# Performance work log

Measured on AMD Instinct MI355X. Metric: run time of the kernel, lower is better.

The kernel has to match this reference:

```python
import jax, jax.numpy as jnp
import numpy as np

B, S, D, H, DFF = 8, 1024, 1024, 16, 4096
DK = D // H
EPS = 1e-5


def layernorm(x, g, b):
    mu = jnp.mean(x, axis=-1, keepdims=True)
    var = jnp.var(x, axis=-1, keepdims=True)
    return (x - mu) * jax.lax.rsqrt(var + EPS) * g + b


def mha(q_in, k_in, v_in, wq, bq, wk, bk, wv, bv, wo, bo):
    # weights stored as [in, out] (transposed torch Linear)
    nb = q_in.shape[0]
    def split(t):  # [B,S,D] -> [B,H,S,DK]
        return t.reshape(nb, -1, H, DK).transpose(0, 2, 1, 3)
    q = split(q_in @ wq + bq)
    k = split(k_in @ wk + bk)
    v = split(v_in @ wv + bv)
    scores = jnp.einsum('bhqd,bhkd->bhqk', q, k) / jnp.sqrt(jnp.float32(DK))
    p = jax.nn.softmax(scores, axis=-1)
    o = jnp.einsum('bhqk,bhkd->bhqd', p, v)
    o = o.transpose(0, 2, 1, 3).reshape(nb, -1, D)
    return o @ wo + bo


def setup_inputs() -> dict:
    key = jax.random.key(0)
    ks = jax.random.split(key, 40)
    i = iter(range(40))
    def rn(shape, scale=1.0):
        return jax.random.normal(ks[next(i)], shape, dtype=jnp.float32) * scale
    d = {}
    d['x'] = rn((B, S, D))
    d['y'] = rn((B, S, D))
    d['x_pos'] = rn((B, S, D))
    d['y_pos'] = rn((B, S, D))
    w_scale = 1.0 / np.sqrt(D)
    for pfx in ('sa', 'ca'):
        for nm in ('q', 'k', 'v', 'o'):
            d[f'{pfx}_w{nm}'] = rn((D, D), w_scale)
            d[f'{pfx}_b{nm}'] = jnp.zeros((D,), jnp.float32)
    d['ffn_w1'] = rn((D, DFF), w_scale)
    d['ffn_b1'] = jnp.zeros((DFF,), jnp.float32)
    d['ffn_w2'] = rn((DFF, D), 1.0 / np.sqrt(DFF))
    d['ffn_b2'] = jnp.zeros((D,), jnp.float32)
    for n in (1, 2, 3, 4):
        d[f'ln{n}_g'] = jnp.ones((D,), jnp.float32)
        d[f'ln{n}_b'] = jnp.zeros((D,), jnp.float32)
    return d


def reference(x, y, x_pos, y_pos,
              sa_wq, sa_bq, sa_wk, sa_bk, sa_wv, sa_bv, sa_wo, sa_bo,
              ca_wq, ca_bq, ca_wk, ca_bk, ca_wv, ca_bv, ca_wo, ca_bo,
              ffn_w1, ffn_b1, ffn_w2, ffn_b2,
              ln1_g, ln1_b, ln2_g, ln2_b, ln3_g, ln3_b, ln4_g, ln4_b):
    # pre-norm variant (norm_before=True), eval mode (dropout=0)
    x2 = layernorm(x, ln1_g, ln1_b)
    qk = x2 + x_pos
    x = x + mha(qk, qk, x2, sa_wq, sa_bq, sa_wk, sa_bk, sa_wv, sa_bv, sa_wo, sa_bo)
    x2 = layernorm(x, ln2_g, ln2_b)
    y2 = layernorm(y, ln3_g, ln3_b)
    x = x + mha(x2 + x_pos, y2 + y_pos, y2,
                ca_wq, ca_bq, ca_wk, ca_bk, ca_wv, ca_bv, ca_wo, ca_bo)
    x2 = layernorm(x, ln4_g, ln4_b)
    h = x2 @ ffn_w1 + ffn_b1
    h = h * jax.nn.sigmoid(h)  # Swish
    return x + (h @ ffn_w2 + ffn_b2)
```

## Files before the change

### kernel.cpp

```cpp
#include <hip/hip_runtime.h>
#include <hip/hip_bf16.h>

#define NB 8
#define NS 1024
#define ND 1024
#define NH 16
#define NDK 64
#define NDFF 4096

typedef __bf16 bf16;
typedef __attribute__((ext_vector_type(8))) __bf16 bf16x8;
typedef __attribute__((ext_vector_type(4))) __bf16 bf16x4;
typedef __attribute__((ext_vector_type(4))) float f32x4;

__device__ __forceinline__ void gload16(const bf16* g, bf16* l) {
  __builtin_amdgcn_global_load_lds(
      (const __attribute__((address_space(1))) void*)g,
      (__attribute__((address_space(3))) void*)l, 16, 0, 0);
}

__global__ void wconv_t(const float* __restrict__ W, bf16* __restrict__ WT,
                        int K, int N) {
  __shared__ float tile[32][33];
  int n0 = blockIdx.x * 32, k0 = blockIdx.y * 32;
  int tx = threadIdx.x, ty = threadIdx.y;
#pragma unroll
  for (int i2 = 0; i2 < 4; ++i2) {
    int i = ty + i2 * 8;
    tile[i][tx] = W[(long)(k0 + i) * N + n0 + tx];
  }
  __syncthreads();
#pragma unroll
  for (int i2 = 0; i2 < 4; ++i2) {
    int i = ty + i2 * 8;
    WT[(long)(n0 + i) * K + k0 + tx] = (bf16)tile[tx][i];
  }
}

__global__ void ln_fused(const float* __restrict__ in, const float* __restrict__ gam,
                         const float* __restrict__ bet, const float* __restrict__ pos,
                         bf16* __restrict__ out_ln, bf16* __restrict__ out_lnpos) {
  long row = blockIdx.x;
  int t = threadIdx.x;
  float4 v = ((const float4*)(in + row * ND))[t];
  float s = v.x + v.y + v.z + v.w;
  float s2 = v.x * v.x + v.y * v.y + v.z * v.z + v.w * v.w;
#pragma unroll
  for (int m = 32; m >= 1; m >>= 1) {
    s += __shfl_xor(s, m);
    s2 += __shfl_xor(s2, m);
  }
  __shared__ float red[8];
  if ((t & 63) == 0) {
    red[t >> 6] = s;
    red[4 + (t >> 6)] = s2;
  }
  __syncthreads();
  float ts = red[0] + red[1] + red[2] + red[3];
  float ts2 = red[4] + red[5] + red[6] + red[7];
  float mu = ts * (1.0f / ND);
  float var = ts2 * (1.0f / ND) - mu * mu;
  float rstd = rsqrtf(var + 1e-5f);
  float4 g4 = ((const float4*)gam)[t];
  float4 b4 = ((const float4*)bet)[t];
  float o0 = (v.x - mu) * rstd * g4.x + b4.x;
  float o1 = (v.y - mu) * rstd * g4.y + b4.y;
  float o2 = (v.z - mu) * rstd * g4.z + b4.z;
  float o3 = (v.w - mu) * rstd * g4.w + b4.w;
  if (out_ln) {
    bf16x4 q;
    q[0] = (bf16)o0; q[1] = (bf16)o1; q[2] = (bf16)o2; q[3] = (bf16)o3;
    *(bf16x4*)(out_ln + row * ND + t * 4) = q;
  }
  if (out_lnpos) {
    float4 p4 = ((const float4*)(pos + row * ND))[t];
    bf16x4 q;
    q[0] = (bf16)(o0 + p4.x); q[1] = (bf16)(o1 + p4.y);
    q[2] = (bf16)(o2 + p4.z); q[3] = (bf16)(o3 + p4.w);
    *(bf16x4*)(out_lnpos + row * ND + t * 4) = q;
  }
}

template <int MODE>
__global__ __launch_bounds__(512, 2) void gemm_bt(
    const bf16* __restrict__ A, const bf16* __restrict__ WT,
    const float* __restrict__ bias, const float* __restrict__ res,
    void* __restrict__ out, int M, int N, int K) {
  __shared__ bf16 SA[5][256 * 32];
  __shared__ bf16 SB[5][128 * 32];
  const int t = threadIdx.x;
  const int w = t >> 6, l = t & 63;
  const int wr = w >> 2, wc = w & 3;
  const int wrm = w >> 1, wcn = w & 1;
  (void)wr; (void)wc;
  const int c = l & 15, g = l >> 4;
  const long row0 = (long)blockIdx.x * 256;
  const long col0 = (long)blockIdx.y * 128;
  const int NT = K >> 5;

  f32x4 acc[4][4];
#pragma unroll
  for (int m = 0; m < 4; ++m)
#pragma unroll
    for (int n = 0; n < 4; ++n) acc[m][n] = (f32x4){0.f, 0.f, 0.f, 0.f};

  const int lr = l >> 2;
  const int lcol = 8 * ((l & 3) ^ ((l >> 3) & 3));
  const bf16* Ag0 = A + (row0 + w * 32 + lr) * (long)K + lcol;
  const bf16* Ag1 = Ag0 + 16 * (long)K;
  const bf16* Bg0 = WT + (col0 + w * 16 + lr) * (long)K + lcol;

#define STAGE(BS, KK)                              \
  do {                                             \
    gload16(Ag0 + (KK), &SA[BS][(w * 32) * 32]);   \
    gload16(Ag1 + (KK), &SA[BS][(w * 32 + 16) * 32]); \
    gload16(Bg0 + (KK), &SB[BS][(w * 16) * 32]);   \
  } while (0)

  STAGE(0, 0);
  STAGE(1, 32);
  STAGE(2, 64);
  STAGE(3, 96);

  const int swz8 = (g ^ ((c >> 1) & 3)) * 8;
  int aoff[4], boff[4];
#pragma unroll
  for (int m = 0; m < 4; ++m) aoff[m] = (wrm * 64 + m * 16 + c) * 32 + swz8;
#pragma unroll
  for (int n = 0; n < 4; ++n) boff[n] = (wcn * 64 + n * 16 + c) * 32 + swz8;

  int cb = 0, sb = 4;
  int ks_off = 128;
  for (int tt = 0; tt < NT; ++tt) {
    const int rem = NT - 1 - tt;
    if (rem >= 3) {
      asm volatile("s_waitcnt vmcnt(9)" ::: "memory");
    } else if (rem == 2) {
      asm volatile("s_waitcnt vmcnt(6)" ::: "memory");
    } else if (rem == 1) {
      asm volatile("s_waitcnt vmcnt(3)" ::: "memory");
    } else {
      asm volatile("s_waitcnt vmcnt(0)" ::: "memory");
    }
    __builtin_amdgcn_s_barrier();

    const int ca = cb * (256 * 32);
    const int cbb = cb * (128 * 32);
    bf16x8 af[4], bfr[4];
#pragma unroll
    for (int m = 0; m < 4; ++m) af[m] = *(const bf16x8*)&SA[0][ca + aoff[m]];
#pragma unroll
    for (int n = 0; n < 4; ++n) bfr[n] = *(const bf16x8*)&SB[0][cbb + boff[n]];

    if (tt + 4 < NT) STAGE(sb, ks_off);

    __builtin_amdgcn_s_barrier();
    __builtin_amdgcn_s_setprio(1);
#pragma unroll
    for (int m = 0; m < 4; ++m)
#pragma unroll
      for (int n = 0; n < 4; ++n)
        acc[m][n] = __builtin_amdgcn_mfma_f32_16x16x32_bf16(af[m], bfr[n], acc[m][n], 0, 0, 0);
    __builtin_amdgcn_s_setprio(0);

    cb = (cb == 4) ? 0 : cb + 1;
    sb = (sb == 4) ? 0 : sb + 1;
    ks_off += 32;
  }
#undef STAGE

#pragma unroll
  for (int n = 0; n < 4; ++n) {
    const long col = col0 + wcn * 64 + n * 16 + c;
    const float bv = bias[col];
#pragma unroll
    for (int m = 0; m < 4; ++m) {
      const long rowb = row0 + wrm * 64 + m * 16 + g * 4;
#pragma unroll
      for (int r = 0; r < 4; ++r) {
        float v = acc[m][n][r] + bv;
        const long idx = (rowb + r) * N + col;
        if (MODE == 0) {
          ((bf16*)out)[idx] = (bf16)v;
        } else if (MODE == 1) {
          ((float*)out)[idx] = res[idx] + v;
        } else {
          float sw = v / (1.f + __expf(-v));
          ((bf16*)out)[idx] = (bf16)sw;
        }
      }
    }
  }
}

__global__ void vtrans(const bf16* __restrict__ V, bf16* __restrict__ VT) {
  __shared__ bf16 tile[32][33];
  int st = blockIdx.x * 32, dt = blockIdx.y * 32;
  int bh = blockIdx.z;
  int b = bh >> 4, h = bh & 15;
  int tx = threadIdx.x, ty = threadIdx.y;
#pragma unroll
  for (int i2 = 0; i2 < 4; ++i2) {
    int i = ty + i2 * 8;
    tile[i][tx] = V[((long)b * NS + st + i) * ND + h * NDK + dt + tx];
  }
  __syncthreads();
#pragma unroll
  for (int i2 = 0; i2 < 4; ++i2) {
    int i = ty + i2 * 8;
    VT[((long)bh * NDK + dt + i) * NS + st + tx] = tile[tx][i];
  }
}

__global__ __launch_bounds__(256) void attn_fwd(
    const bf16* __restrict__ Q, const bf16* __restrict__ Kt,
    const bf16* __restrict__ VT, bf16* __restrict__ O) {
  __shared__ bf16 Ks[2][64 * 64];
  __shared__ bf16 Vs[2][64 * 64];
  __shared__ bf16 Pl[4][2][16 * 68];
  int t = threadIdx.x;
  int w = t >> 6, l = t & 63;
  int c = l & 15, g = l >> 4;
  int bid = blockIdx.x;
  int qt = bid >> 7, bh = bid & 127;
  int b = bh >> 4, h = bh & 15;
  int q0 = qt * 128 + w * 32;
  int swz = (c & 7) << 4;

  bf16x8 qf[2][2];
  const bf16* Qbase = Q + (long)(b * NS) * ND + h * NDK;
#pragma unroll
  for (int sj = 0; sj < 2; ++sj) {
    const bf16* qr = Qbase + (long)(q0 + sj * 16 + c) * ND + g * 8;
    qf[sj][0] = *(const bf16x8*)qr;
    qf[sj][1] = *(const bf16x8*)(qr + 32);
  }

  const bf16* Kg = Kt + (long)(b * NS) * ND + h * NDK;
  const bf16* Vg = VT + (long)(b * NH + h) * NDK * NS;

  int sr = l >> 3;
  int sc8 = 8 * ((l & 7) ^ sr);

  f32x4 o[2][4];
#pragma unroll
  for (int sj = 0; sj < 2; ++sj)
#pragma unroll
    for (int ds = 0; ds < 4; ++ds) o[sj][ds] = (f32x4){0.f, 0.f, 0.f, 0.f};
  float mx[2] = {-1e30f, -1e30f};
  float lsum[2] = {0.f, 0.f};

#define STAGE(BUF, KV)                                                        \
  {                                                                           \
    _Pragma("unroll") for (int j = 0; j < 2; ++j) {                           \
      int row = w * 16 + j * 8 + sr;                                          \
      gload16(Kg + (long)((KV) + row) * ND + sc8,                             \
              &Ks[BUF][(w * 16 + j * 8) * 64]);                               \
      gload16(Vg + (long)row * NS + (KV) + sc8,                               \
              &Vs[BUF][(w * 16 + j * 8) * 64]);                               \
    }                                                                         \
  }

  STAGE(0, 0);
  asm volatile("s_waitcnt vmcnt(0)" ::: "memory");
  __syncthreads();

  int buf = 0;
  for (int it = 0; it < NS / 64; ++it) {
    if (it + 1 < NS / 64) STAGE(buf ^ 1, (it + 1) * 64);

    f32x4 sv[2][4];
#pragma unroll
    for (int sj = 0; sj < 2; ++sj)
#pragma unroll
      for (int kt = 0; kt < 4; ++kt) sv[sj][kt] = (f32x4){0.f, 0.f, 0.f, 0.f};
    __builtin_amdgcn_s_setprio(1);
#pragma unroll
    for (int kt = 0; kt < 4; ++kt) {
      const char* kr = (const char*)&Ks[buf][(kt * 16 + c) * 64];
      bf16x8 ka0 = *(const bf16x8*)(kr + ((g * 16) ^ swz));
      bf16x8 ka1 = *(const bf16x8*)(kr + ((64 + g * 16) ^ swz));
#pragma unroll
      for (int sj = 0; sj < 2; ++sj) {
        sv[sj][kt] = __builtin_amdgcn_mfma_f32_16x16x32_bf16(ka0, qf[sj][0], sv[sj][kt], 0, 0, 0);
        sv[sj][kt] = __builtin_amdgcn_mfma_f32_16x16x32_bf16(ka1, qf[sj][1], sv[sj][kt], 0, 0, 0);
      }
    }
    __builtin_amdgcn_s_setprio(0);

    float pm[2];
#pragma unroll
    for (int sj = 0; sj < 2; ++sj) {
      float m = -1e30f;
#pragma unroll
      for (int kt = 0; kt < 4; ++kt)
#pragma unroll
        for (int r = 0; r < 4; ++r) {
          sv[sj][kt][r] *= 0.125f;
          m = fmaxf(m, sv[sj][kt][r]);
        }
      m = fmaxf(m, __shfl_xor(m, 16));
      m = fmaxf(m, __shfl_xor(m, 32));
      pm[sj] = m;
    }
    int cond = (pm[0] <= mx[0] + 8.f) && (pm[1] <= mx[1] + 8.f);
    if (!__all(cond)) {
#pragma unroll
      for (int sj = 0; sj < 2; ++sj) {
        float mn = fmaxf(mx[sj], pm[sj]);
        float sc = __expf(mx[sj] - mn);
        mx[sj] = mn;
        lsum[sj] *= sc;
#pragma unroll
        for (int ds = 0; ds < 4; ++ds)
#pragma unroll
          for (int r = 0; r < 4; ++r) o[sj][ds][r] *= sc;
      }
    }
#pragma unroll
    for (int sj = 0; sj < 2; ++sj) {
      float rs = 0.f;
#pragma unroll
      for (int kt = 0; kt < 4; ++kt) {
        bf16x4 pw;
#pragma unroll
        for (int r = 0; r < 4; ++r) {
          float e = __expf(sv[sj][kt][r] - mx[sj]);
          rs += e;
          pw[r] = (bf16)e;
        }
        *(bf16x4*)&Pl[w][sj][c * 68 + kt * 16 + 4 * g] = pw;
      }
      rs += __shfl_xor(rs, 16);
      rs += __shfl_xor(rs, 32);
      lsum[sj] += rs;
    }
    asm volatile("s_waitcnt lgkmcnt(0)" ::: "memory");
    __builtin_amdgcn_sched_barrier(0);

    __builtin_amdgcn_s_setprio(1);
#pragma unroll
    for (int ks = 0; ks < 2; ++ks) {
      bf16x8 pb0 = *(const bf16x8*)&Pl[w][0][c * 68 + ks * 32 + g * 8];
      bf16x8 pb1 = *(const bf16x8*)&Pl[w][1][c * 68 + ks * 32 + g * 8];
#pragma unroll
      for (int ds = 0; ds < 4; ++ds) {
        const char* vr = (const char*)&Vs[buf][(ds * 16 + c) * 64];
        bf16x8 va = *(const bf16x8*)(vr + ((ks * 64 + g * 16) ^ swz));
        o[0][ds] = __builtin_amdgcn_mfma_f32_16x16x32_bf16(va, pb0, o[0][ds], 0, 0, 0);
        o[1][ds] = __builtin_amdgcn_mfma_f32_16x16x32_bf16(va, pb1, o[1][ds], 0, 0, 0);
      }
    }
    __builtin_amdgcn_s_setprio(0);
    __syncthreads();
    buf ^= 1;
  }

#pragma unroll
  for (int sj = 0; sj < 2; ++sj) {
    float inv = 1.f / lsum[sj];
    bf16* Orow = O + (long)(b * NS + q0 + sj * 16 + c) * ND + h * NDK;
#pragma unroll
    for (int ds = 0; ds < 4; ++ds) {
      bf16x4 ov;
#pragma unroll
      for (int r = 0; r < 4; ++r) ov[r] = (bf16)(o[sj][ds][r] * inv);
      *(bf16x4*)(Orow + ds * 16 + 4 * g) = ov;
    }
  }
#undef STAGE
}

extern "C" void kernel_launch(void* const* d_in, const int* in_sizes, int n_in,
                              void* d_out, int out_size, void* d_ws, size_t ws_size,
                              hipStream_t stream) {
  (void)in_sizes; (void)n_in; (void)out_size; (void)ws_size;
  const float* x = (const float*)d_in[0];
  const float* y = (const float*)d_in[1];
  const float* x_pos = (const float*)d_in[2];
  const float* y_pos = (const float*)d_in[3];

  char* ws = (char*)d_ws;
  const size_t MB = 1ull << 20;
  bf16* Wt[8];
  for (int i = 0; i < 8; ++i) Wt[i] = (bf16*)(ws + (size_t)i * 2 * MB);
  bf16* W1T = (bf16*)(ws + 16 * MB);
  bf16* W2T = (bf16*)(ws + 24 * MB);
  float* xres = (float*)(ws + 32 * MB);
  bf16* x2 = (bf16*)(ws + 64 * MB);
  bf16* qk = (bf16*)(ws + 80 * MB);
  bf16* y2 = (bf16*)(ws + 96 * MB);
  bf16* yk = (bf16*)(ws + 112 * MB);
  bf16* Qb = (bf16*)(ws + 128 * MB);
  bf16* Kb = (bf16*)(ws + 144 * MB);
  bf16* Vb = (bf16*)(ws + 160 * MB);
  bf16* VTb = (bf16*)(ws + 176 * MB);
  bf16* Ob = (bf16*)(ws + 192 * MB);
  bf16* hb = (bf16*)(ws + 128 * MB);

  dim3 tb(32, 8);
  for (int i = 0; i < 8; ++i)
    wconv_t<<<dim3(32, 32), tb, 0, stream>>>((const float*)d_in[4 + 2 * i], Wt[i], 1024, 1024);
  wconv_t<<<dim3(128, 32), tb, 0, stream>>>((const float*)d_in[20], W1T, 1024, 4096);
  wconv_t<<<dim3(32, 128), tb, 0, stream>>>((const float*)d_in[22], W2T, 4096, 1024);

  const float* ln1g = (const float*)d_in[24]; const float* ln1b = (const float*)d_in[25];
  const float* ln2g = (const float*)d_in[26]; const float* ln2b = (const float*)d_in[27];
  const float* ln3g = (const float*)d_in[28]; const float* ln3b = (const float*)d_in[29];
  const float* ln4g = (const float*)d_in[30]; const float* ln4b = (const float*)d_in[31];

  dim3 gD(32, 8);
  dim3 gF1(32, 32);
  dim3 gVT(32, 2, 128);

  ln_fused<<<8192, 256, 0, stream>>>(x, ln1g, ln1b, x_pos, x2, qk);
  gemm_bt<0><<<gD, 512, 0, stream>>>(qk, Wt[0], (const float*)d_in[5], nullptr, Qb, 8192, 1024, 1024);
  gemm_bt<0><<<gD, 512, 0, stream>>>(qk, Wt[1], (const float*)d_in[7], nullptr, Kb, 8192, 1024, 1024);
  gemm_bt<0><<<gD, 512, 0, stream>>>(x2, Wt[2], (const float*)d_in[9], nullptr, Vb, 8192, 1024, 1024);
  vtrans<<<gVT, tb, 0, stream>>>(Vb, VTb);
  attn_fwd<<<1024, 256, 0, stream>>>(Qb, Kb, VTb, Ob);
  gemm_bt<1><<<gD, 512, 0, stream>>>(Ob, Wt[3], (const float*)d_in[11], x, xres, 8192, 1024, 1024);

  ln_fused<<<8192, 256, 0, stream>>>(xres, ln2g, ln2b, x_pos, nullptr, qk);
  ln_fused<<<8192, 256, 0, stream>>>(y, ln3g, ln3b, y_pos, y2, yk);
  gemm_bt<0><<<gD, 512, 0, stream>>>(qk, Wt[4], (const float*)d_in[13], nullptr, Qb, 8192, 1024, 1024);
  gemm_bt<0><<<gD, 512, 0, stream>>>(yk, Wt[5], (const float*)d_in[15], nullptr, Kb, 8192, 1024, 1024);
  gemm_bt<0><<<gD, 512, 0, stream>>>(y2, Wt[6], (const float*)d_in[17], nullptr, Vb, 8192, 1024, 1024);
  vtrans<<<gVT, tb, 0, stream>>>(Vb, VTb);
  attn_fwd<<<1024, 256, 0, stream>>>(Qb, Kb, VTb, Ob);
  gemm_bt<1><<<gD, 512, 0, stream>>>(Ob, Wt[7], (const float*)d_in[19], xres, xres, 8192, 1024, 1024);

  ln_fused<<<8192, 256, 0, stream>>>(xres, ln4g, ln4b, nullptr, x2, nullptr);
  gemm_bt<2><<<gF1, 512, 0, stream>>>(x2, W1T, (const float*)d_in[21], nullptr, hb, 8192, 4096, 1024);
  gemm_bt<1><<<gD, 512, 0, stream>>>(hb, W2T, (const float*)d_in[23], xres, (float*)d_out, 8192, 1024, 4096);
}
```

Baseline: 698.8 us.

## Shrink GEMM block tile to 128x128 with 4 waves and drop a barrier

The bf16 GEMM now uses 256-thread blocks computing 128x128 tiles instead of 512-thread blocks computing 256x128 tiles, which doubles the grid size for every projection and FFN GEMM. Each wave now issues four 16-byte global-to-LDS loads per stage, and the vmcnt thresholds are rescaled to match. The next-stage prefetch is issued right after the single barrier, before the LDS fragment reads, and the second per-iteration barrier is removed. The LDS swizzle is changed to fit the new load pattern. Smaller tiles mean less data reuse per block, in exchange for more blocks per CU to spread load and hide latency.

```diff
diff --git a/kernel.cpp b/kernel.cpp
--- a/kernel.cpp
+++ b/kernel.cpp
@@ -82,19 +82,17 @@
 }
 
 template <int MODE>
-__global__ __launch_bounds__(512, 2) void gemm_bt(
+__global__ __launch_bounds__(256, 2) void gemm_bt(
     const bf16* __restrict__ A, const bf16* __restrict__ WT,
     const float* __restrict__ bias, const float* __restrict__ res,
     void* __restrict__ out, int M, int N, int K) {
-  __shared__ bf16 SA[5][256 * 32];
+  __shared__ bf16 SA[5][128 * 32];
   __shared__ bf16 SB[5][128 * 32];
   const int t = threadIdx.x;
   const int w = t >> 6, l = t & 63;
-  const int wr = w >> 2, wc = w & 3;
-  const int wrm = w >> 1, wcn = w & 1;
-  (void)wr; (void)wc;
+  const int wr = w >> 1, wc = w & 1;
   const int c = l & 15, g = l >> 4;
-  const long row0 = (long)blockIdx.x * 256;
+  const long row0 = (long)blockIdx.x * 128;
   const long col0 = (long)blockIdx.y * 128;
   const int NT = K >> 5;
 
@@ -104,17 +102,21 @@
 #pragma unroll
     for (int n = 0; n < 4; ++n) acc[m][n] = (f32x4){0.f, 0.f, 0.f, 0.f};
 
-  const int lr = l >> 2;
-  const int lcol = 8 * ((l & 3) ^ ((l >> 3) & 3));
-  const bf16* Ag0 = A + (row0 + w * 32 + lr) * (long)K + lcol;
-  const bf16* Ag1 = Ag0 + 16 * (long)K;
-  const bf16* Bg0 = WT + (col0 + w * 16 + lr) * (long)K + lcol;
-
-#define STAGE(BS, KK)                              \
-  do {                                             \
-    gload16(Ag0 + (KK), &SA[BS][(w * 32) * 32]);   \
-    gload16(Ag1 + (KK), &SA[BS][(w * 32 + 16) * 32]); \
-    gload16(Bg0 + (KK), &SB[BS][(w * 16) * 32]);   \
+  const int srow = l >> 2;
+  const int schunk = 8 * ((l & 3) ^ (srow & 3));
+  const bf16* Ag0 = A + (row0 + w * 16 + srow) * (long)K + schunk;
+  const bf16* Ag1 = Ag0 + 64 * (long)K;
+  const bf16* Bg0 = WT + (col0 + w * 16 + srow) * (long)K + schunk;
+  const bf16* Bg1 = Bg0 + 64 * (long)K;
+  bf16* const SAf = &SA[0][0];
+  bf16* const SBf = &SB[0][0];
+
+#define STAGE(SL, KK)                                  \
+  do {                                                 \
+    gload16(Ag0 + (KK), SAf + (SL) * 4096 + (w * 16) * 32);        \
+    gload16(Ag1 + (KK), SAf + (SL) * 4096 + (64 + w * 16) * 32);   \
+    gload16(Bg0 + (KK), SBf + (SL) * 4096 + (w * 16) * 32);        \
+    gload16(Bg1 + (KK), SBf + (SL) * 4096 + (64 + w * 16) * 32);   \
   } while (0)
 
   STAGE(0, 0);
@@ -122,39 +124,37 @@
   STAGE(2, 64);
   STAGE(3, 96);
 
-  const int swz8 = (g ^ ((c >> 1) & 3)) * 8;
+  const int rsw = (g ^ (c & 3)) * 8;
   int aoff[4], boff[4];
 #pragma unroll
-  for (int m = 0; m < 4; ++m) aoff[m] = (wrm * 64 + m * 16 + c) * 32 + swz8;
-#pragma unroll
-  for (int n = 0; n < 4; ++n) boff[n] = (wcn * 64 + n * 16 + c) * 32 + swz8;
+  for (int m = 0; m < 4; ++m) aoff[m] = (wr * 64 + m * 16 + c) * 32 + rsw;
+#pragma unroll
+  for (int n = 0; n < 4; ++n) boff[n] = (wc * 64 + n * 16 + c) * 32 + rsw;
 
   int cb = 0, sb = 4;
-  int ks_off = 128;
+  int kst = 128;
   for (int tt = 0; tt < NT; ++tt) {
     const int rem = NT - 1 - tt;
     if (rem >= 3) {
-      asm volatile("s_waitcnt vmcnt(9)" ::: "memory");
+      asm volatile("s_waitcnt vmcnt(12)" ::: "memory");
     } else if (rem == 2) {
-      asm volatile("s_waitcnt vmcnt(6)" ::: "memory");
+      asm volatile("s_waitcnt vmcnt(8)" ::: "memory");
     } else if (rem == 1) {
-      asm volatile("s_waitcnt vmcnt(3)" ::: "memory");
+      asm volatile("s_waitcnt vmcnt(4)" ::: "memory");
     } else {
       asm volatile("s_waitcnt vmcnt(0)" ::: "memory");
     }
     __builtin_amdgcn_s_barrier();
 
-    const int ca = cb * (256 * 32);
-    const int cbb = cb * (128 * 32);
+    if (tt + 4 < NT) STAGE(sb, kst);
+
+    const int ca = cb * 4096;
     bf16x8 af[4], bfr[4];
 #pragma unroll
-    for (int m = 0; m < 4; ++m) af[m] = *(const bf16x8*)&SA[0][ca + aoff[m]];
-#pragma unroll
-    for (int n = 0; n < 4; ++n) bfr[n] = *(const bf16x8*)&SB[0][cbb + boff[n]];
-
-    if (tt + 4 < NT) STAGE(sb, ks_off);
-
-    __builtin_amdgcn_s_barrier();
+    for (int m = 0; m < 4; ++m) af[m] = *(const bf16x8*)(SAf + ca + aoff[m]);
+#pragma unroll
+    for (int n = 0; n < 4; ++n) bfr[n] = *(const bf16x8*)(SBf + ca + boff[n]);
+
     __builtin_amdgcn_s_setprio(1);
 #pragma unroll
     for (int m = 0; m < 4; ++m)
@@ -165,17 +165,17 @@
 
     cb = (cb == 4) ? 0 : cb + 1;
     sb = (sb == 4) ? 0 : sb + 1;
-    ks_off += 32;
+    kst += 32;
   }
 #undef STAGE
 
 #pragma unroll
   for (int n = 0; n < 4; ++n) {
-    const long col = col0 + wcn * 64 + n * 16 + c;
+    const long col = col0 + wc * 64 + n * 16 + c;
     const float bv = bias[col];
 #pragma unroll
     for (int m = 0; m < 4; ++m) {
-      const long rowb = row0 + wrm * 64 + m * 16 + g * 4;
+      const long rowb = row0 + wr * 64 + m * 16 + g * 4;
 #pragma unroll
       for (int r = 0; r < 4; ++r) {
         float v = acc[m][n][r] + bv;
@@ -409,28 +409,28 @@
   const float* ln3g = (const float*)d_in[28]; const float* ln3b = (const float*)d_in[29];
   const float* ln4g = (const float*)d_in[30]; const float* ln4b = (const float*)d_in[31];
 
-  dim3 gD(32, 8);
-  dim3 gF1(32, 32);
+  dim3 gD(64, 8);
+  dim3 gF1(64, 32);
   dim3 gVT(32, 2, 128);
 
   ln_fused<<<8192, 256, 0, stream>>>(x, ln1g, ln1b, x_pos, x2, qk);
-  gemm_bt<0><<<gD, 512, 0, stream>>>(qk, Wt[0], (const float*)d_in[5], nullptr, Qb, 8192, 1024, 1024);
-  gemm_bt<0><<<gD, 512, 0, stream>>>(qk, Wt[1], (const float*)d_in[7], nullptr, Kb, 8192, 1024, 1024);
-  gemm_bt<0><<<gD, 512, 0, stream>>>(x2, Wt[2], (const float*)d_in[9], nullptr, Vb, 8192, 1024, 1024);
+  gemm_bt<0><<<gD, 256, 0, stream>>>(qk, Wt[0], (const float*)d_in[5], nullptr, Qb, 8192, 1024, 1024);
+  gemm_bt<0><<<gD, 256, 0, stream>>>(qk, Wt[1], (const float*)d_in[7], nullptr, Kb, 8192, 1024, 1024);
+  gemm_bt<0><<<gD, 256, 0, stream>>>(x2, Wt[2], (const float*)d_in[9], nullptr, Vb, 8192, 1024, 1024);
   vtrans<<<gVT, tb, 0, stream>>>(Vb, VTb);
   attn_fwd<<<1024, 256, 0, stream>>>(Qb, Kb, VTb, Ob);
-  gemm_bt<1><<<gD, 512, 0, stream>>>(Ob, Wt[3], (const float*)d_in[11], x, xres, 8192, 1024, 1024);
+  gemm_bt<1><<<gD, 256, 0, stream>>>(Ob, Wt[3], (const float*)d_in[11], x, xres, 8192, 1024, 1024);
 
   ln_fused<<<8192, 256, 0, stream>>>(xres, ln2g, ln2b, x_pos, nullptr, qk);
   ln_fused<<<8192, 256, 0, stream>>>(y, ln3g, ln3b, y_pos, y2, yk);
-  gemm_bt<0><<<gD, 512, 0, stream>>>(qk, Wt[4], (const float*)d_in[13], nullptr, Qb, 8192, 1024, 1024);
-  gemm_bt<0><<<gD, 512, 0, stream>>>(yk, Wt[5], (const float*)d_in[15], nullptr, Kb, 8192, 1024, 1024);
-  gemm_bt<0><<<gD, 512, 0, stream>>>(y2, Wt[6], (const float*)d_in[17], nullptr, Vb, 8192, 1024, 1024);
+  gemm_bt<0><<<gD, 256, 0, stream>>>(qk, Wt[4], (const float*)d_in[13], nullptr, Qb, 8192, 1024, 1024);
+  gemm_bt<0><<<gD, 256, 0, stream>>>(yk, Wt[5], (const float*)d_in[15], nullptr, Kb, 8192, 1024, 1024);
+  gemm_bt<0><<<gD, 256, 0, stream>>>(y2, Wt[6], (const float*)d_in[17], nullptr, Vb, 8192, 1024, 1024);
   vtrans<<<gVT, tb, 0, stream>>>(Vb, VTb);
   attn_fwd<<<1024, 256, 0, stream>>>(Qb, Kb, VTb, Ob);
-  gemm_bt<1><<<gD, 512, 0, stream>>>(Ob, Wt[7], (const float*)d_in[19], xres, xres, 8192, 1024, 1024);
+  gemm_bt<1><<<gD, 256, 0, stream>>>(Ob, Wt[7], (const float*)d_in[19], xres, xres, 8192, 1024, 1024);
 
   ln_fused<<<8192, 256, 0, stream>>>(xres, ln4g, ln4b, nullptr, x2, nullptr);
-  gemm_bt<2><<<gF1, 512, 0, stream>>>(x2, W1T, (const float*)d_in[21], nullptr, hb, 8192, 4096, 1024);
-  gemm_bt<1><<<gD, 512, 0, stream>>>(hb, W2T, (const float*)d_in[23], xres, (float*)d_out, 8192, 1024, 4096);
-}
+  gemm_bt<2><<<gF1, 256, 0, stream>>>(x2, W1T, (const float*)d_in[21], nullptr, hb, 8192, 4096, 1024);
+  gemm_bt<1><<<gD, 256, 0, stream>>>(hb, W2T, (const float*)d_in[23], xres, (float*)d_out, 8192, 1024, 4096);
+}
```

After: 764.6 us. +9.4%, slower.

## Reshape GEMM warp tiling to 8x2 and shorten LDS pipeline depth

Applied to the files above, without the earlier changes.

Changes the per-warp tile from 4x4 MFMA blocks (wave grid 4x2) to 8x2 blocks (wave grid 2x4) and shrinks the LDS ring from five stages with prefetch distance four to four stages with prefetch distance two. It also adds explicit lgkmcnt waits and a sched_barrier before the MFMA loop, and lowers launch bounds to one block per CU. The intent is to cut the LDS footprint and simplify synchronization. The 8x2 tile reads more LDS fragments per MFMA than 4x4 (10 vs 8 for 16 MFMAs), the shallower prefetch exposes more global latency, and the launch-bound change may reduce occupancy.

```diff
diff --git a/kernel.cpp b/kernel.cpp
--- a/kernel.cpp
+++ b/kernel.cpp
@@ -82,100 +82,89 @@
 }
 
 template <int MODE>
-__global__ __launch_bounds__(512, 2) void gemm_bt(
+__global__ __launch_bounds__(512, 1) void gemm_bt(
     const bf16* __restrict__ A, const bf16* __restrict__ WT,
     const float* __restrict__ bias, const float* __restrict__ res,
     void* __restrict__ out, int M, int N, int K) {
-  __shared__ bf16 SA[5][256 * 32];
-  __shared__ bf16 SB[5][128 * 32];
+  __shared__ bf16 SA[4][256 * 32];
+  __shared__ bf16 SB[4][128 * 32];
   const int t = threadIdx.x;
   const int w = t >> 6, l = t & 63;
-  const int wr = w >> 2, wc = w & 3;
-  const int wrm = w >> 1, wcn = w & 1;
-  (void)wr; (void)wc;
+  const int wr = w >> 2;
+  const int wc = w & 3;
   const int c = l & 15, g = l >> 4;
   const long row0 = (long)blockIdx.x * 256;
   const long col0 = (long)blockIdx.y * 128;
   const int NT = K >> 5;
 
-  f32x4 acc[4][4];
-#pragma unroll
-  for (int m = 0; m < 4; ++m)
-#pragma unroll
-    for (int n = 0; n < 4; ++n) acc[m][n] = (f32x4){0.f, 0.f, 0.f, 0.f};
-
-  const int lr = l >> 2;
-  const int lcol = 8 * ((l & 3) ^ ((l >> 3) & 3));
-  const bf16* Ag0 = A + (row0 + w * 32 + lr) * (long)K + lcol;
-  const bf16* Ag1 = Ag0 + 16 * (long)K;
-  const bf16* Bg0 = WT + (col0 + w * 16 + lr) * (long)K + lcol;
-
-#define STAGE(BS, KK)                              \
-  do {                                             \
-    gload16(Ag0 + (KK), &SA[BS][(w * 32) * 32]);   \
-    gload16(Ag1 + (KK), &SA[BS][(w * 32 + 16) * 32]); \
-    gload16(Bg0 + (KK), &SB[BS][(w * 16) * 32]);   \
+  f32x4 acc[8][2];
+#pragma unroll
+  for (int m = 0; m < 8; ++m)
+#pragma unroll
+    for (int n = 0; n < 2; ++n) acc[m][n] = (f32x4){0.f, 0.f, 0.f, 0.f};
+
+  const int srow = l >> 2;
+  const int sslot = 8 * ((l & 3) ^ ((l >> 3) & 3));
+  const bf16* AgA = A + (row0 + w * 16 + srow) * (long)K + sslot;
+  const bf16* AgB = A + (row0 + 128 + w * 16 + srow) * (long)K + sslot;
+  const bf16* BgA = WT + (col0 + w * 16 + srow) * (long)K + sslot;
+
+#define STAGE(SL, KK)                                      \
+  do {                                                     \
+    gload16(AgA + (KK), &SA[SL][(w * 16) * 32]);           \
+    gload16(AgB + (KK), &SA[SL][(128 + w * 16) * 32]);     \
+    gload16(BgA + (KK), &SB[SL][(w * 16) * 32]);           \
   } while (0)
+
+  const int rsw = (g ^ ((c >> 1) & 3)) * 8;
+  int aoff[8], boff[2];
+#pragma unroll
+  for (int m = 0; m < 8; ++m) aoff[m] = (wr * 128 + m * 16 + c) * 32 + rsw;
+#pragma unroll
+  for (int n = 0; n < 2; ++n) boff[n] = (wc * 32 + n * 16 + c) * 32 + rsw;
 
   STAGE(0, 0);
   STAGE(1, 32);
-  STAGE(2, 64);
-  STAGE(3, 96);
-
-  const int swz8 = (g ^ ((c >> 1) & 3)) * 8;
-  int aoff[4], boff[4];
-#pragma unroll
-  for (int m = 0; m < 4; ++m) aoff[m] = (wrm * 64 + m * 16 + c) * 32 + swz8;
-#pragma unroll
-  for (int n = 0; n < 4; ++n) boff[n] = (wcn * 64 + n * 16 + c) * 32 + swz8;
-
-  int cb = 0, sb = 4;
-  int ks_off = 128;
+  asm volatile("s_waitcnt vmcnt(3)" ::: "memory");
+  __builtin_amdgcn_s_barrier();
+
   for (int tt = 0; tt < NT; ++tt) {
-    const int rem = NT - 1 - tt;
-    if (rem >= 3) {
-      asm volatile("s_waitcnt vmcnt(9)" ::: "memory");
-    } else if (rem == 2) {
-      asm volatile("s_waitcnt vmcnt(6)" ::: "memory");
-    } else if (rem == 1) {
+    const int cb = tt & 3;
+    bf16x8 af[8], bfr[2];
+#pragma unroll
+    for (int m = 0; m < 8; ++m) af[m] = *(const bf16x8*)&SA[cb][aoff[m]];
+#pragma unroll
+    for (int n = 0; n < 2; ++n) bfr[n] = *(const bf16x8*)&SB[cb][boff[n]];
+
+    if (tt + 2 < NT) STAGE((tt + 2) & 3, (tt + 2) << 5);
+
+    __builtin_amdgcn_s_barrier();
+    asm volatile("s_waitcnt lgkmcnt(0)" ::: "memory");
+    __builtin_amdgcn_sched_barrier(0);
+    __builtin_amdgcn_s_setprio(1);
+#pragma unroll
+    for (int m = 0; m < 8; ++m)
+#pragma unroll
+      for (int n = 0; n < 2; ++n)
+        acc[m][n] = __builtin_amdgcn_mfma_f32_16x16x32_bf16(af[m], bfr[n], acc[m][n], 0, 0, 0);
+    __builtin_amdgcn_s_setprio(0);
+
+    if (tt + 2 < NT) {
       asm volatile("s_waitcnt vmcnt(3)" ::: "memory");
     } else {
       asm volatile("s_waitcnt vmcnt(0)" ::: "memory");
     }
     __builtin_amdgcn_s_barrier();
-
-    const int ca = cb * (256 * 32);
-    const int cbb = cb * (128 * 32);
-    bf16x8 af[4], bfr[4];
-#pragma unroll
-    for (int m = 0; m < 4; ++m) af[m] = *(const bf16x8*)&SA[0][ca + aoff[m]];
-#pragma unroll
-    for (int n = 0; n < 4; ++n) bfr[n] = *(const bf16x8*)&SB[0][cbb + boff[n]];
-
-    if (tt + 4 < NT) STAGE(sb, ks_off);
-
-    __builtin_amdgcn_s_barrier();
-    __builtin_amdgcn_s_setprio(1);
-#pragma unroll
-    for (int m = 0; m < 4; ++m)
-#pragma unroll
-      for (int n = 0; n < 4; ++n)
-        acc[m][n] = __builtin_amdgcn_mfma_f32_16x16x32_bf16(af[m], bfr[n], acc[m][n], 0, 0, 0);
-    __builtin_amdgcn_s_setprio(0);
-
-    cb = (cb == 4) ? 0 : cb + 1;
-    sb = (sb == 4) ? 0 : sb + 1;
-    ks_off += 32;
   }
 #undef STAGE
 
 #pragma unroll
-  for (int n = 0; n < 4; ++n) {
-    const long col = col0 + wcn * 64 + n * 16 + c;
+  for (int n = 0; n < 2; ++n) {
+    const long col = col0 + wc * 32 + n * 16 + c;
     const float bv = bias[col];
 #pragma unroll
-    for (int m = 0; m < 4; ++m) {
-      const long rowb = row0 + wrm * 64 + m * 16 + g * 4;
+    for (int m = 0; m < 8; ++m) {
+      const long rowb = row0 + wr * 128 + m * 16 + g * 4;
 #pragma unroll
       for (int r = 0; r < 4; ++r) {
         float v = acc[m][n][r] + bv;
```

Measured after the change: 717.2 us. +2.6%, slower.
